# Optimization experiments

Measured on AMD Instinct MI355X. Metric: run time of the kernel, lower is better.

The kernel has to match this reference:

```python
import jax, jax.numpy as jnp
import numpy as np

B, H, T, D = 4, 16, 2048, 64


def setup_inputs() -> dict:
    key = jax.random.key(0)
    kq, kk, kv = jax.random.split(key, 3)
    q = jax.random.normal(kq, (B, H, T, D), dtype=jnp.float32)
    k = jax.random.normal(kk, (B, H, T, D), dtype=jnp.float32)
    v = jax.random.normal(kv, (B, H, T, D), dtype=jnp.float32)
    return {"q": q, "k": k, "v": v}


def reference(q, k, v):
    # scores: [B,H,T,T] = q @ k^T (no softmax, linear attention)
    scores = jnp.einsum("bhtd,bhsd->bhts", q, k)
    # causal multiplicative mask: lower-triangular ones (zero out future keys)
    t = q.shape[-2]
    causal = jnp.tril(jnp.ones((t, t), dtype=scores.dtype))  # [T,T]
    scores = scores * causal  # broadcast over [B,H]
    # output: [B,H,T,D] = masked_scores @ v
    return jnp.einsum("bhts,bhsd->bhtd", scores, v)
```

## Files before the change

kernel.cpp:

```cpp
#include <hip/hip_runtime.h>
#include <hip/hip_bf16.h>


#define B_   4
#define H_   16
#define T_   2048
#define D_   64
#define BH_  64
#define CCH  256
#define NCH  8
#define LPAD 8
#define LW   (D_ + LPAD)

typedef __bf16 bf16x4 __attribute__((ext_vector_type(4)));
typedef __bf16 bf16x8 __attribute__((ext_vector_type(8)));
typedef float  f32x4  __attribute__((ext_vector_type(4)));


__global__ __launch_bounds__(256, 2) void kv_chunk_kernel(
    const float* __restrict__ k, const float* __restrict__ v,
    float* __restrict__ kvws) {
  __shared__ __align__(16) __bf16 KT[2][D_][LW];
  __shared__ __align__(16) __bf16 VT[2][D_][LW];

  const int tid  = threadIdx.x;
  const int lane = tid & 63;
  const int w    = tid >> 6;
  const int quad = lane >> 4;
  const int l15  = lane & 15;
  const int bh   = blockIdx.x >> 3;
  const int c    = blockIdx.x & (NCH - 1);
  const long base = ((long)bh * T_ + (long)c * CCH) * D_;

  const int s4 = tid >> 4;
  const int d4 = tid & 15;

  f32x4 kreg[4], vreg[4];
  const float* kp0 = k + base + (long)(s4 * 4) * D_ + d4 * 4;
  const float* vp0 = v + base + (long)(s4 * 4) * D_ + d4 * 4;

  auto LOAD = [&](int st) {
#pragma unroll
    for (int r = 0; r < 4; ++r) {
      kreg[r] = *(const f32x4*)(kp0 + (long)(st * 64 + r) * D_);
      vreg[r] = *(const f32x4*)(vp0 + (long)(st * 64 + r) * D_);
    }
  };
  auto WRITE = [&](int p) {
#pragma unroll
    for (int cc2 = 0; cc2 < 4; ++cc2) {
      bf16x4 ka, va;
#pragma unroll
      for (int r = 0; r < 4; ++r) {
        ka[r] = (__bf16)kreg[r][cc2];
        va[r] = (__bf16)vreg[r][cc2];
      }
      *(bf16x4*)&KT[p][d4 * 4 + cc2][s4 * 4] = ka;
      *(bf16x4*)&VT[p][d4 * 4 + cc2][s4 * 4] = va;
    }
  };

  const f32x4 vzero = {0.f, 0.f, 0.f, 0.f};
  f32x4 acc[4];
#pragma unroll
  for (int n = 0; n < 4; ++n) acc[n] = vzero;

  LOAD(0);
  WRITE(0);
  __syncthreads();
  for (int st = 0; st < 4; ++st) {
    const int p = st & 1;
    if (st < 3) LOAD(st + 1);
#pragma unroll
    for (int ks = 0; ks < 2; ++ks) {
      bf16x8 a = *(const bf16x8*)&KT[p][w * 16 + l15][ks * 32 + quad * 8];
#pragma unroll
      for (int n = 0; n < 4; ++n) {
        bf16x8 b = *(const bf16x8*)&VT[p][n * 16 + l15][ks * 32 + quad * 8];
        acc[n] = __builtin_amdgcn_mfma_f32_16x16x32_bf16(a, b, acc[n], 0, 0, 0);
      }
    }
    if (st < 3) {
      WRITE(p ^ 1);
      __syncthreads();
    }
  }
  float* out = kvws + ((long)blockIdx.x << 12);
#pragma unroll
  for (int n = 0; n < 4; ++n)
#pragma unroll
    for (int rr = 0; rr < 4; ++rr)
      out[(w * 16 + quad * 4 + rr) * 64 + n * 16 + l15] = acc[n][rr];
}

__global__ __launch_bounds__(256, 2) void attn_chunk_kernel(
    const float* __restrict__ q, const float* __restrict__ k,
    const float* __restrict__ v, const float* __restrict__ kvws,
    float* __restrict__ out) {
  __shared__ __align__(16) __bf16 KVT[D_][LW];
  __shared__ __align__(16) __bf16 Kj[2][64][LW];
  __shared__ __align__(16) __bf16 VTj[2][D_][LW];
  __shared__ __align__(16) __bf16 Sw[4][16][LW];

  const int tid  = threadIdx.x;
  const int lane = tid & 63;
  const int w    = tid >> 6;
  const int quad = lane >> 4;
  const int l15  = lane & 15;
  const int bh   = blockIdx.x >> 3;
  const int c    = blockIdx.x & (NCH - 1);
  const long base = ((long)bh * T_ + (long)c * CCH) * D_;

  const int slK = tid >> 2;
  const int d0K = (tid & 3) * 16;
  const int s4  = tid >> 4;
  const int d4  = tid & 15;

  f32x4 kreg[4], vreg[4];
  auto LOADJ = [&](int j) {
    const float* kp = k + base + (long)(j * 64 + slK) * D_ + d0K;
    const float* vp = v + base + (long)(j * 64 + s4 * 4) * D_ + d4 * 4;
#pragma unroll
    for (int r = 0; r < 4; ++r) kreg[r] = *(const f32x4*)(kp + r * 4);
#pragma unroll
    for (int r = 0; r < 4; ++r) vreg[r] = *(const f32x4*)(vp + (long)r * D_);
  };
  auto WRITEJ = [&](int p) {
    bf16x8 kb0, kb1;
#pragma unroll
    for (int e = 0; e < 4; ++e) {
      kb0[e]     = (__bf16)kreg[0][e];
      kb0[4 + e] = (__bf16)kreg[1][e];
      kb1[e]     = (__bf16)kreg[2][e];
      kb1[4 + e] = (__bf16)kreg[3][e];
    }
    *(bf16x8*)&Kj[p][slK][d0K]     = kb0;
    *(bf16x8*)&Kj[p][slK][d0K + 8] = kb1;
#pragma unroll
    for (int cc2 = 0; cc2 < 4; ++cc2) {
      bf16x4 va;
#pragma unroll
      for (int r = 0; r < 4; ++r) va[r] = (__bf16)vreg[r][cc2];
      *(bf16x4*)&VTj[p][d4 * 4 + cc2][s4 * 4] = va;
    }
  };

  float kvacc[16];
#pragma unroll
  for (int i = 0; i < 16; ++i) kvacc[i] = 0.f;
  const float* wsbh = kvws + ((long)(bh * NCH) << 12);
  for (int cc = 0; cc < c; ++cc) {
    const float* pp = wsbh + ((long)cc << 12) + tid * 16;
#pragma unroll
    for (int x = 0; x < 4; ++x) {
      f32x4 t = *(const f32x4*)(pp + x * 4);
#pragma unroll
      for (int e = 0; e < 4; ++e) kvacc[x * 4 + e] += t[e];
    }
  }
  {
    const int d1  = tid >> 2;
    const int d2b = (tid & 3) * 16;
#pragma unroll
    for (int ii = 0; ii < 16; ++ii) KVT[d2b + ii][d1] = (__bf16)kvacc[ii];
  }

  bf16x8 qf[4][2];
#pragma unroll
  for (int i = 0; i < 4; ++i) {
    int row = (w + 4 * i) * 16 + l15;
    const float* qp = q + base + (long)row * D_ + quad * 8;
#pragma unroll
    for (int ks = 0; ks < 2; ++ks) {
      f32x4 lo = *(const f32x4*)(qp + ks * 32);
      f32x4 hi = *(const f32x4*)(qp + ks * 32 + 4);
      bf16x8 f;
#pragma unroll
      for (int e = 0; e < 4; ++e) {
        f[e]     = (__bf16)lo[e];
        f[4 + e] = (__bf16)hi[e];
      }
      qf[i][ks] = f;
    }
  }

  const f32x4 vzero = {0.f, 0.f, 0.f, 0.f};
  f32x4 acc[4][4];
#pragma unroll
  for (int i = 0; i < 4; ++i)
#pragma unroll
    for (int n = 0; n < 4; ++n) acc[i][n] = vzero;

  LOADJ(0);
  WRITEJ(0);
  __syncthreads();
  LOADJ(1);

#pragma unroll
  for (int ks = 0; ks < 2; ++ks)
#pragma unroll
    for (int n = 0; n < 4; ++n) {
      bf16x8 b = *(const bf16x8*)&KVT[n * 16 + l15][ks * 32 + quad * 8];
#pragma unroll
      for (int i = 0; i < 4; ++i)
        acc[i][n] =
            __builtin_amdgcn_mfma_f32_16x16x32_bf16(qf[i][ks], b, acc[i][n], 0, 0, 0);
    }

  for (int j = 0; j < 4; ++j) {
    const int p = j & 1;
    bf16x8 kfrag[2][4], vfrag[2][4];
#pragma unroll
    for (int ks = 0; ks < 2; ++ks)
#pragma unroll
      for (int n = 0; n < 4; ++n) {
        kfrag[ks][n] = *(const bf16x8*)&Kj[p][n * 16 + l15][ks * 32 + quad * 8];
        vfrag[ks][n] = *(const bf16x8*)&VTj[p][n * 16 + l15][ks * 32 + quad * 8];
      }
    for (int i = j; i < 4; ++i) {
      f32x4 s[4];
#pragma unroll
      for (int n = 0; n < 4; ++n) s[n] = vzero;
#pragma unroll
      for (int ks = 0; ks < 2; ++ks)
#pragma unroll
        for (int n = 0; n < 4; ++n)
          s[n] = __builtin_amdgcn_mfma_f32_16x16x32_bf16(kfrag[ks][n], qf[i][ks],
                                                         s[n], 0, 0, 0);
#pragma unroll
      for (int n = 0; n < 4; ++n) {
        bf16x4 pk;
#pragma unroll
        for (int rr = 0; rr < 4; ++rr) {
          float val = s[n][rr];
          if (i == j && (n * 16 + quad * 4 + rr > 16 * w + l15)) val = 0.f;
          pk[rr] = (__bf16)val;
        }
        *(bf16x4*)&Sw[w][l15][n * 16 + quad * 4] = pk;
      }
#pragma unroll
      for (int ks = 0; ks < 2; ++ks) {
        bf16x8 a = *(const bf16x8*)&Sw[w][l15][ks * 32 + quad * 8];
#pragma unroll
        for (int n = 0; n < 4; ++n)
          acc[i][n] =
              __builtin_amdgcn_mfma_f32_16x16x32_bf16(a, vfrag[ks][n], acc[i][n], 0, 0, 0);
      }
    }
    if (j < 3) {
      WRITEJ(p ^ 1);
      __syncthreads();
      if (j < 2) LOADJ(j + 2);
    }
  }

  float* op = out + base;
#pragma unroll
  for (int i = 0; i < 4; ++i) {
    int row = (w + 4 * i) * 16 + quad * 4;
#pragma unroll
    for (int n = 0; n < 4; ++n)
#pragma unroll
      for (int rr = 0; rr < 4; ++rr)
        op[(long)(row + rr) * D_ + n * 16 + l15] = acc[i][n][rr];
  }
}

extern "C" void kernel_launch(void* const* d_in, const int* in_sizes, int n_in,
                              void* d_out, int out_size, void* d_ws, size_t ws_size,
                              hipStream_t stream) {
  const float* q = (const float*)d_in[0];
  const float* k = (const float*)d_in[1];
  const float* v = (const float*)d_in[2];
  float* out = (float*)d_out;
  float* kvws = (float*)d_ws;

  hipLaunchKernelGGL(kv_chunk_kernel, dim3(BH_ * NCH), dim3(256), 0, stream,
                     k, v, kvws);
  hipLaunchKernelGGL(attn_chunk_kernel, dim3(BH_ * NCH), dim3(256), 0, stream,
                     q, k, v, kvws, out);
}
```

Before: 143.7 us.

## Use 8 waves per block in attention kernel with balanced causal row pairing

The attention chunk kernel now runs 512 threads (8 waves) instead of 256, and each wave owns two 16-row query tiles paired as m and 15-m. The old mapping gave each wave four tiles with uneven causal work, so the pairing evens out the triangular load across waves. K and V fragments are now read from LDS inside the loop instead of being held in registers, which lowers register pressure so more waves fit per CU. The cost is more LDS reads per MFMA, and launch bounds now request 512 threads with 4 blocks.

```diff
diff --git a/kernel.cpp b/kernel.cpp
--- a/kernel.cpp
+++ b/kernel.cpp
@@ -14,6 +14,7 @@
 
 typedef __bf16 bf16x4 __attribute__((ext_vector_type(4)));
 typedef __bf16 bf16x8 __attribute__((ext_vector_type(8)));
+typedef float  f32x2  __attribute__((ext_vector_type(2)));
 typedef float  f32x4  __attribute__((ext_vector_type(4)));
 
 
@@ -93,14 +94,14 @@
       out[(w * 16 + quad * 4 + rr) * 64 + n * 16 + l15] = acc[n][rr];
 }
 
-__global__ __launch_bounds__(256, 2) void attn_chunk_kernel(
+__global__ __launch_bounds__(512, 4) void attn_chunk_kernel(
     const float* __restrict__ q, const float* __restrict__ k,
     const float* __restrict__ v, const float* __restrict__ kvws,
     float* __restrict__ out) {
   __shared__ __align__(16) __bf16 KVT[D_][LW];
   __shared__ __align__(16) __bf16 Kj[2][64][LW];
   __shared__ __align__(16) __bf16 VTj[2][D_][LW];
-  __shared__ __align__(16) __bf16 Sw[4][16][LW];
+  __shared__ __align__(16) __bf16 Sw[8][16][LW];
 
   const int tid  = threadIdx.x;
   const int lane = tid & 63;
@@ -111,64 +112,63 @@
   const int c    = blockIdx.x & (NCH - 1);
   const long base = ((long)bh * T_ + (long)c * CCH) * D_;
 
-  const int slK = tid >> 2;
-  const int d0K = (tid & 3) * 16;
-  const int s4  = tid >> 4;
-  const int d4  = tid & 15;
-
-  f32x4 kreg[4], vreg[4];
+  const int slK = tid >> 3;
+  const int d0K = (tid & 7) * 8;
+  const int sV  = (tid >> 5) * 4;
+  const int dV  = (tid & 31) * 2;
+
+  f32x4 kreg0, kreg1;
+  f32x2 vreg[4];
   auto LOADJ = [&](int j) {
     const float* kp = k + base + (long)(j * 64 + slK) * D_ + d0K;
-    const float* vp = v + base + (long)(j * 64 + s4 * 4) * D_ + d4 * 4;
-#pragma unroll
-    for (int r = 0; r < 4; ++r) kreg[r] = *(const f32x4*)(kp + r * 4);
-#pragma unroll
-    for (int r = 0; r < 4; ++r) vreg[r] = *(const f32x4*)(vp + (long)r * D_);
+    const float* vp = v + base + (long)(j * 64 + sV) * D_ + dV;
+    kreg0 = *(const f32x4*)(kp);
+    kreg1 = *(const f32x4*)(kp + 4);
+#pragma unroll
+    for (int r = 0; r < 4; ++r) vreg[r] = *(const f32x2*)(vp + (long)r * D_);
   };
   auto WRITEJ = [&](int p) {
-    bf16x8 kb0, kb1;
+    bf16x8 kb;
 #pragma unroll
     for (int e = 0; e < 4; ++e) {
-      kb0[e]     = (__bf16)kreg[0][e];
-      kb0[4 + e] = (__bf16)kreg[1][e];
-      kb1[e]     = (__bf16)kreg[2][e];
-      kb1[4 + e] = (__bf16)kreg[3][e];
-    }
-    *(bf16x8*)&Kj[p][slK][d0K]     = kb0;
-    *(bf16x8*)&Kj[p][slK][d0K + 8] = kb1;
-#pragma unroll
-    for (int cc2 = 0; cc2 < 4; ++cc2) {
+      kb[e]     = (__bf16)kreg0[e];
+      kb[4 + e] = (__bf16)kreg1[e];
+    }
+    *(bf16x8*)&Kj[p][slK][d0K] = kb;
+#pragma unroll
+    for (int e = 0; e < 2; ++e) {
       bf16x4 va;
 #pragma unroll
-      for (int r = 0; r < 4; ++r) va[r] = (__bf16)vreg[r][cc2];
-      *(bf16x4*)&VTj[p][d4 * 4 + cc2][s4 * 4] = va;
-    }
-  };
-
-  float kvacc[16];
-#pragma unroll
-  for (int i = 0; i < 16; ++i) kvacc[i] = 0.f;
+      for (int r = 0; r < 4; ++r) va[r] = (__bf16)vreg[r][e];
+      *(bf16x4*)&VTj[p][dV + e][sV] = va;
+    }
+  };
+
+  float kvacc[8];
+#pragma unroll
+  for (int i = 0; i < 8; ++i) kvacc[i] = 0.f;
   const float* wsbh = kvws + ((long)(bh * NCH) << 12);
   for (int cc = 0; cc < c; ++cc) {
-    const float* pp = wsbh + ((long)cc << 12) + tid * 16;
-#pragma unroll
-    for (int x = 0; x < 4; ++x) {
+    const float* pp = wsbh + ((long)cc << 12) + tid * 8;
+#pragma unroll
+    for (int x = 0; x < 2; ++x) {
       f32x4 t = *(const f32x4*)(pp + x * 4);
 #pragma unroll
       for (int e = 0; e < 4; ++e) kvacc[x * 4 + e] += t[e];
     }
   }
   {
-    const int d1  = tid >> 2;
-    const int d2b = (tid & 3) * 16;
-#pragma unroll
-    for (int ii = 0; ii < 16; ++ii) KVT[d2b + ii][d1] = (__bf16)kvacc[ii];
-  }
-
-  bf16x8 qf[4][2];
-#pragma unroll
-  for (int i = 0; i < 4; ++i) {
-    int row = (w + 4 * i) * 16 + l15;
+    const int d1  = tid >> 3;
+    const int d2b = (tid & 7) * 8;
+#pragma unroll
+    for (int ii = 0; ii < 8; ++ii) KVT[d2b + ii][d1] = (__bf16)kvacc[ii];
+  }
+
+  bf16x8 qf[2][2];
+#pragma unroll
+  for (int t = 0; t < 2; ++t) {
+    const int m = t ? (15 - w) : w;
+    const int row = m * 16 + l15;
     const float* qp = q + base + (long)row * D_ + quad * 8;
 #pragma unroll
     for (int ks = 0; ks < 2; ++ks) {
@@ -180,16 +180,16 @@
         f[e]     = (__bf16)lo[e];
         f[4 + e] = (__bf16)hi[e];
       }
-      qf[i][ks] = f;
+      qf[t][ks] = f;
     }
   }
 
   const f32x4 vzero = {0.f, 0.f, 0.f, 0.f};
-  f32x4 acc[4][4];
-#pragma unroll
-  for (int i = 0; i < 4; ++i)
-#pragma unroll
-    for (int n = 0; n < 4; ++n) acc[i][n] = vzero;
+  f32x4 acc[2][4];
+#pragma unroll
+  for (int t = 0; t < 2; ++t)
+#pragma unroll
+    for (int n = 0; n < 4; ++n) acc[t][n] = vzero;
 
   LOADJ(0);
   WRITEJ(0);
@@ -202,49 +202,51 @@
     for (int n = 0; n < 4; ++n) {
       bf16x8 b = *(const bf16x8*)&KVT[n * 16 + l15][ks * 32 + quad * 8];
 #pragma unroll
-      for (int i = 0; i < 4; ++i)
-        acc[i][n] =
-            __builtin_amdgcn_mfma_f32_16x16x32_bf16(qf[i][ks], b, acc[i][n], 0, 0, 0);
+      for (int t = 0; t < 2; ++t)
+        acc[t][n] =
+            __builtin_amdgcn_mfma_f32_16x16x32_bf16(qf[t][ks], b, acc[t][n], 0, 0, 0);
     }
 
   for (int j = 0; j < 4; ++j) {
     const int p = j & 1;
-    bf16x8 kfrag[2][4], vfrag[2][4];
-#pragma unroll
-    for (int ks = 0; ks < 2; ++ks)
-#pragma unroll
-      for (int n = 0; n < 4; ++n) {
-        kfrag[ks][n] = *(const bf16x8*)&Kj[p][n * 16 + l15][ks * 32 + quad * 8];
-        vfrag[ks][n] = *(const bf16x8*)&VTj[p][n * 16 + l15][ks * 32 + quad * 8];
-      }
-    for (int i = j; i < 4; ++i) {
-      f32x4 s[4];
-#pragma unroll
-      for (int n = 0; n < 4; ++n) s[n] = vzero;
-#pragma unroll
-      for (int ks = 0; ks < 2; ++ks)
-#pragma unroll
-        for (int n = 0; n < 4; ++n)
-          s[n] = __builtin_amdgcn_mfma_f32_16x16x32_bf16(kfrag[ks][n], qf[i][ks],
-                                                         s[n], 0, 0, 0);
-#pragma unroll
-      for (int n = 0; n < 4; ++n) {
-        bf16x4 pk;
-#pragma unroll
-        for (int rr = 0; rr < 4; ++rr) {
-          float val = s[n][rr];
-          if (i == j && (n * 16 + quad * 4 + rr > 16 * w + l15)) val = 0.f;
-          pk[rr] = (__bf16)val;
+#pragma unroll
+    for (int t = 0; t < 2; ++t) {
+      const int m = t ? (15 - w) : w;
+      if (m >= 4 * j) {
+        f32x4 s[4];
+#pragma unroll
+        for (int n = 0; n < 4; ++n) s[n] = vzero;
+#pragma unroll
+        for (int ks = 0; ks < 2; ++ks)
+#pragma unroll
+          for (int n = 0; n < 4; ++n) {
+            bf16x8 kf = *(const bf16x8*)&Kj[p][n * 16 + l15][ks * 32 + quad * 8];
+            s[n] = __builtin_amdgcn_mfma_f32_16x16x32_bf16(kf, qf[t][ks], s[n],
+                                                           0, 0, 0);
+          }
+        const int mloc = (m & 3) * 16;
+        const bool diag = ((m >> 2) == j);
+#pragma unroll
+        for (int n = 0; n < 4; ++n) {
+          bf16x4 pk;
+#pragma unroll
+          for (int rr = 0; rr < 4; ++rr) {
+            float val = s[n][rr];
+            if (diag && (n * 16 + quad * 4 + rr > mloc + l15)) val = 0.f;
+            pk[rr] = (__bf16)val;
+          }
+          *(bf16x4*)&Sw[w][l15][n * 16 + quad * 4] = pk;
         }
-        *(bf16x4*)&Sw[w][l15][n * 16 + quad * 4] = pk;
-      }
-#pragma unroll
-      for (int ks = 0; ks < 2; ++ks) {
-        bf16x8 a = *(const bf16x8*)&Sw[w][l15][ks * 32 + quad * 8];
-#pragma unroll
-        for (int n = 0; n < 4; ++n)
-          acc[i][n] =
-              __builtin_amdgcn_mfma_f32_16x16x32_bf16(a, vfrag[ks][n], acc[i][n], 0, 0, 0);
+#pragma unroll
+        for (int ks = 0; ks < 2; ++ks) {
+          bf16x8 a = *(const bf16x8*)&Sw[w][l15][ks * 32 + quad * 8];
+#pragma unroll
+          for (int n = 0; n < 4; ++n) {
+            bf16x8 vf = *(const bf16x8*)&VTj[p][n * 16 + l15][ks * 32 + quad * 8];
+            acc[t][n] =
+                __builtin_amdgcn_mfma_f32_16x16x32_bf16(a, vf, acc[t][n], 0, 0, 0);
+          }
+        }
       }
     }
     if (j < 3) {
@@ -256,13 +258,14 @@
 
   float* op = out + base;
 #pragma unroll
-  for (int i = 0; i < 4; ++i) {
-    int row = (w + 4 * i) * 16 + quad * 4;
+  for (int t = 0; t < 2; ++t) {
+    const int m = t ? (15 - w) : w;
+    const int row = m * 16 + quad * 4;
 #pragma unroll
     for (int n = 0; n < 4; ++n)
 #pragma unroll
       for (int rr = 0; rr < 4; ++rr)
-        op[(long)(row + rr) * D_ + n * 16 + l15] = acc[i][n][rr];
+        op[(long)(row + rr) * D_ + n * 16 + l15] = acc[t][n][rr];
   }
 }
 
@@ -277,6 +280,6 @@
 
   hipLaunchKernelGGL(kv_chunk_kernel, dim3(BH_ * NCH), dim3(256), 0, stream,
                      k, v, kvws);
-  hipLaunchKernelGGL(attn_chunk_kernel, dim3(BH_ * NCH), dim3(256), 0, stream,
+  hipLaunchKernelGGL(attn_chunk_kernel, dim3(BH_ * NCH), dim3(512), 0, stream,
                      q, k, v, kvws, out);
 }
```

Measured after the change: 146.5 us. About the same (+1.9%).
